# Optimization experiments

Measured on AMD Instinct MI355X. Metric: run time of the kernel, lower is better.

The kernel has to match this reference:

```python
import math
import jax, jax.numpy as jnp
import numpy as np

N_HEADS = 16

def setup_inputs() -> dict:
    key = jax.random.key(0)
    qkv = jax.random.normal(key, (4, 3072, 2048), dtype=jnp.float32)
    return {"qkv": qkv}

def reference(qkv):
    bs, width, length = qkv.shape
    ch = width // (3 * N_HEADS)
    # [bs*H, 3*ch, L] -> split into q, k, v of [bs*H, ch, L]
    qkv_r = qkv.reshape(bs * N_HEADS, 3 * ch, length)
    q, k, v = qkv_r[:, :ch], qkv_r[:, ch:2 * ch], qkv_r[:, 2 * ch:]
    scale = 1.0 / math.sqrt(math.sqrt(ch))
    # scores: [bs*H, T, S]
    weight = jnp.einsum('bct,bcs->bts', q * scale, k * scale)
    weight = jax.nn.softmax(weight, axis=-1)
    a = jnp.einsum('bts,bcs->bct', weight, v)
    return a.reshape(bs, -1, length)
```

## Files before the change

kernel.cpp:

```cpp
#include <hip/hip_runtime.h>
#include <cstdint>

typedef _Float16 half8 __attribute__((ext_vector_type(8)));
typedef __fp16 fp16x2 __attribute__((ext_vector_type(2)));
typedef float f32x4 __attribute__((ext_vector_type(4)));

#define HSTRIDE 131072
#define KOFF    ((size_t)64 * HSTRIDE)
#define VOFF    ((size_t)128 * HSTRIDE)

__device__ __forceinline__ float fast_exp2(float x) {
    return __builtin_amdgcn_exp2f(x);
}

__device__ __forceinline__ uint32_t pkrtz(float a, float b) {
    fp16x2 h = __builtin_amdgcn_cvt_pkrtz(a, b);
    return __builtin_bit_cast(uint32_t, h);
}

__device__ __forceinline__ void load_lds16(const _Float16* g, _Float16* l) {
    auto* g1 = reinterpret_cast<const __attribute__((address_space(1))) uint32_t*>(
        reinterpret_cast<uintptr_t>(g));
    auto* l3 = reinterpret_cast<__attribute__((address_space(3))) uint32_t*>(
        reinterpret_cast<uintptr_t>(l));
    __builtin_amdgcn_global_load_lds(g1, l3, 16, 0, 0);
}

__global__ __launch_bounds__(256) void prep_kernel(const float* __restrict__ qkv,
                                                   _Float16* __restrict__ ws)
{
    __shared__ float Lf[64 * 132];

    const int tid = threadIdx.x;
    const int bid = blockIdx.x;
    const float kQ = 0.125f * 1.44269504088896340736f;

    if (bid < 2048) {
        const int type  = bid >> 10;
        const int head  = (bid >> 4) & 63;
        const int chunk = bid & 15;
        const int b4 = head >> 4, h = head & 15;
        const float* src = qkv + (((size_t)(b4 * 3072 + h * 192 + type * 64)) << 11)
                         + chunk * 128;

#pragma unroll
        for (int k = 0; k < 8; ++k) {
            int idx = k * 256 + tid;
            int c = idx >> 5;
            int t4 = (idx & 31) << 2;
            *(float4*)&Lf[c * 132 + t4] = *(const float4*)&src[((size_t)c << 11) + t4];
        }
        __syncthreads();

        const int tl = tid >> 1;
        const int gh = (tid & 1) * 4;
        const float scale = (type == 0) ? kQ : 1.0f;
        const int row = chunk * 128 + tl;
        const size_t rowbase = ((type == 0) ? (size_t)head * HSTRIDE
                                            : KOFF + (size_t)head * HSTRIDE)
                             + (size_t)row * 64;
#pragma unroll
        for (int gg = 0; gg < 4; ++gg) {
            const int g = gh + gg;
            uint32_t d[4];
#pragma unroll
            for (int j = 0; j < 4; ++j) {
                float a = Lf[(8 * g + 2 * j) * 132 + tl];
                float b = Lf[(8 * g + 2 * j + 1) * 132 + tl];
                d[j] = pkrtz(a * scale, b * scale);
            }
            const int pos = (type == 0) ? g : (g ^ (tl & 7));
            *(uint4*)&ws[rowbase + ((size_t)pos << 3)] = make_uint4(d[0], d[1], d[2], d[3]);
        }
    } else {
        const int vb = bid - 2048;
        const int head = vb >> 4, chunk = vb & 15;
        const int b4 = head >> 4, h = head & 15;
        const float* src = qkv + (((size_t)(b4 * 3072 + h * 192 + 128)) << 11) + chunk * 128;
#pragma unroll
        for (int k = 0; k < 4; ++k) {
            const int c  = k * 16 + (tid >> 4);
            const int gs = tid & 15;
            const float* p = &src[((size_t)c << 11) + gs * 8];
            float4 f0 = *(const float4*)&p[0];
            float4 f1 = *(const float4*)&p[4];
            uint32_t d0 = pkrtz(f0.x, f0.y);
            uint32_t d1 = pkrtz(f0.z, f0.w);
            uint32_t d2 = pkrtz(f1.x, f1.y);
            uint32_t d3 = pkrtz(f1.z, f1.w);
            size_t o = VOFF + (size_t)head * HSTRIDE + (size_t)chunk * 8192
                     + ((size_t)c << 7) + (size_t)((gs ^ (c & 15)) << 3);
            *(uint4*)&ws[o] = make_uint4(d0, d1, d2, d3);
        }
    }
}

__launch_bounds__(256, 2)
__global__ void attn_kernel(const _Float16* __restrict__ ws, float* __restrict__ out)
{
    __shared__ __align__(16) _Float16 sK[128 * 64];
    __shared__ __align__(16) _Float16 sV[64 * 128];
    __shared__ __align__(16) _Float16 sP[128 * 128];
    __shared__ float sL[4][32];

    const int tid  = threadIdx.x;
    const int lane = tid & 63;
    const int wave = tid >> 6;
    const int l15  = lane & 15;
    const int quad = lane >> 4;

    const int bid  = blockIdx.x;
    const int head = bid & 63;
    const int tblk = bid >> 6;
    const int T0   = tblk * 128;
    const int b4   = head >> 4;
    const int h    = head & 15;

    const _Float16* Qt = ws + (size_t)head * HSTRIDE;
    const _Float16* Kt = ws + KOFF + (size_t)head * HSTRIDE;
    const _Float16* Vt = ws + VOFF + (size_t)head * HSTRIDE;

    half8 qb[2][2];
#pragma unroll
    for (int nt = 0; nt < 2; ++nt)
#pragma unroll
        for (int ks = 0; ks < 2; ++ks)
            qb[nt][ks] = *(const half8*)&Qt[(size_t)(T0 + wave * 32 + nt * 16 + l15) * 64
                                            + ks * 32 + quad * 8];

    int kb[2];
#pragma unroll
    for (int ks = 0; ks < 2; ++ks)
        kb[ks] = l15 * 64 + (((ks * 4 + quad) ^ (l15 & 7)) << 3);
    int vbs[4], pb[4];
#pragma unroll
    for (int ks = 0; ks < 4; ++ks) {
        vbs[ks] = l15 * 128 + (((ks * 4 + quad) ^ l15) << 3);
        pb[ks]  = (wave * 32 + l15) * 128 + (((ks * 4 + quad) ^ l15) << 3);
    }
    int pw[8];
#pragma unroll
    for (int mt = 0; mt < 8; ++mt)
        pw[mt] = (wave * 32 + l15) * 128
               + ((((2 * mt + (quad >> 1)) ^ l15) << 3) + ((quad & 1) << 2));

    f32x4 Oacc[2][4];
#pragma unroll
    for (int nt = 0; nt < 2; ++nt)
#pragma unroll
        for (int ct = 0; ct < 4; ++ct) Oacc[nt][ct] = (f32x4)0.f;
    float lacc[2] = {0.f, 0.f};
    const f32x4 fz = (f32x4)0.f;

    for (int it = 0; it < 16; ++it) {
        __syncthreads();
        const _Float16* kg = Kt + (size_t)it * 8192;
        const _Float16* vg = Vt + (size_t)it * 8192;
#pragma unroll
        for (int i = 0; i < 4; ++i) {
            int off = (i * 4 + wave) * 512;
            load_lds16(kg + off + lane * 8, &sK[off]);
            load_lds16(vg + off + lane * 8, &sV[off]);
        }
        __syncthreads();

        f32x4 Sc[8][2];
#pragma unroll
        for (int mt = 0; mt < 8; ++mt) {
            half8 ka0 = *(const half8*)&sK[kb[0] + mt * 1024];
            half8 ka1 = *(const half8*)&sK[kb[1] + mt * 1024];
#pragma unroll
            for (int nt = 0; nt < 2; ++nt) {
                f32x4 c0 = __builtin_amdgcn_mfma_f32_16x16x32_f16(ka0, qb[nt][0], fz, 0, 0, 0);
                Sc[mt][nt] = __builtin_amdgcn_mfma_f32_16x16x32_f16(ka1, qb[nt][1], c0, 0, 0, 0);
            }
        }

#pragma unroll
        for (int mt = 0; mt < 8; ++mt)
#pragma unroll
            for (int nt = 0; nt < 2; ++nt) {
                f32x4 s = Sc[mt][nt];
                float p0 = fast_exp2(s[0]);
                float p1 = fast_exp2(s[1]);
                float p2 = fast_exp2(s[2]);
                float p3 = fast_exp2(s[3]);
                lacc[nt] += p0; lacc[nt] += p1; lacc[nt] += p2; lacc[nt] += p3;
                uint32_t w0 = pkrtz(p0, p1);
                uint32_t w1 = pkrtz(p2, p3);
                *(uint2*)&sP[pw[mt] + nt * 2048] = make_uint2(w0, w1);
            }

        half8 pa[2][4];
#pragma unroll
        for (int nt = 0; nt < 2; ++nt)
#pragma unroll
            for (int ks = 0; ks < 4; ++ks)
                pa[nt][ks] = *(const half8*)&sP[pb[ks] + nt * 2048];
#pragma unroll
        for (int ct = 0; ct < 4; ++ct) {
#pragma unroll
            for (int ks = 0; ks < 4; ++ks) {
                half8 vbf = *(const half8*)&sV[vbs[ks] + ct * 2048];
                Oacc[0][ct] = __builtin_amdgcn_mfma_f32_16x16x32_f16(pa[0][ks], vbf, Oacc[0][ct], 0, 0, 0);
                Oacc[1][ct] = __builtin_amdgcn_mfma_f32_16x16x32_f16(pa[1][ks], vbf, Oacc[1][ct], 0, 0, 0);
            }
        }
    }

#pragma unroll
    for (int nt = 0; nt < 2; ++nt) {
        float v = lacc[nt];
        v += __shfl_xor(v, 16, 64);
        v += __shfl_xor(v, 32, 64);
        if (quad == 0) sL[wave][nt * 16 + l15] = v;
    }
    __builtin_amdgcn_s_waitcnt(0);
    float inv[2][4];
#pragma unroll
    for (int nt = 0; nt < 2; ++nt)
#pragma unroll
        for (int r = 0; r < 4; ++r)
            inv[nt][r] = 1.f / sL[wave][nt * 16 + quad * 4 + r];

    float* ob = out + (((size_t)(b4 * 1024 + h * 64)) << 11) + T0 + wave * 32;
#pragma unroll
    for (int nt = 0; nt < 2; ++nt)
#pragma unroll
        for (int ct = 0; ct < 4; ++ct) {
            f32x4 o = Oacc[nt][ct];
#pragma unroll
            for (int r = 0; r < 4; ++r) o[r] *= inv[nt][r];
            *(f32x4*)&ob[((size_t)(ct * 16 + l15) << 11) + nt * 16 + quad * 4] = o;
        }
}

extern "C" void kernel_launch(void* const* d_in, const int* in_sizes, int n_in,
                              void* d_out, int out_size, void* d_ws, size_t ws_size,
                              hipStream_t stream) {
    const float* qkv = (const float*)d_in[0];
    float* out = (float*)d_out;
    _Float16* ws = (_Float16*)d_ws;
    prep_kernel<<<dim3(3072), dim3(256), 0, stream>>>(qkv, ws);
    attn_kernel<<<dim3(1024), dim3(256), 0, stream>>>(ws, out);
}
```

Baseline: 252.0 us.

## Double-buffer 64-key K/V tiles in LDS and shrink tiles for higher occupancy

Splits each 128-key iteration into two 64-key halves with double-buffered K and V LDS tiles, so the async global-to-LDS load of the next tile overlaps compute on the current one. The V workspace layout is reorganised into 64-key chunks with a new swizzle to match. The P buffer is halved and read back via two 8-byte loads per fragment. Launch bounds are raised to 3 blocks per CU, now that LDS use is smaller. This trades extra barriers and smaller MFMA batches per barrier for latency hiding and occupancy, at the risk of register spills.

```diff
diff --git a/kernel.cpp b/kernel.cpp
--- a/kernel.cpp
+++ b/kernel.cpp
@@ -88,19 +88,21 @@
             uint32_t d1 = pkrtz(f0.z, f0.w);
             uint32_t d2 = pkrtz(f1.x, f1.y);
             uint32_t d3 = pkrtz(f1.z, f1.w);
-            size_t o = VOFF + (size_t)head * HSTRIDE + (size_t)chunk * 8192
-                     + ((size_t)c << 7) + (size_t)((gs ^ (c & 15)) << 3);
+            const int sch = chunk * 2 + (gs >> 3);
+            const int gsl = gs & 7;
+            size_t o = VOFF + (size_t)head * HSTRIDE + (size_t)sch * 4096
+                     + ((size_t)c << 6) + (size_t)((gsl ^ (c & 7)) << 3);
             *(uint4*)&ws[o] = make_uint4(d0, d1, d2, d3);
         }
     }
 }
 
-__launch_bounds__(256, 2)
+__launch_bounds__(256, 3)
 __global__ void attn_kernel(const _Float16* __restrict__ ws, float* __restrict__ out)
 {
-    __shared__ __align__(16) _Float16 sK[128 * 64];
-    __shared__ __align__(16) _Float16 sV[64 * 128];
-    __shared__ __align__(16) _Float16 sP[128 * 128];
+    __shared__ __align__(16) _Float16 sK[2][4096];
+    __shared__ __align__(16) _Float16 sV[2][4096];
+    __shared__ __align__(16) _Float16 sP[128 * 64];
     __shared__ float sL[4][32];
 
     const int tid  = threadIdx.x;
@@ -128,21 +130,23 @@
             qb[nt][ks] = *(const half8*)&Qt[(size_t)(T0 + wave * 32 + nt * 16 + l15) * 64
                                             + ks * 32 + quad * 8];
 
-    int kb[2];
-#pragma unroll
-    for (int ks = 0; ks < 2; ++ks)
-        kb[ks] = l15 * 64 + (((ks * 4 + quad) ^ (l15 & 7)) << 3);
-    int vbs[4], pb[4];
-#pragma unroll
-    for (int ks = 0; ks < 4; ++ks) {
-        vbs[ks] = l15 * 128 + (((ks * 4 + quad) ^ l15) << 3);
-        pb[ks]  = (wave * 32 + l15) * 128 + (((ks * 4 + quad) ^ l15) << 3);
-    }
-    int pw[8];
-#pragma unroll
-    for (int mt = 0; mt < 8; ++mt)
-        pw[mt] = (wave * 32 + l15) * 128
-               + ((((2 * mt + (quad >> 1)) ^ l15) << 3) + ((quad & 1) << 2));
+    int kb[2], vbs[2];
+#pragma unroll
+    for (int ks = 0; ks < 2; ++ks) {
+        kb[ks]  = l15 * 64 + (((ks * 4 + quad) ^ (l15 & 7)) << 3);
+        vbs[ks] = l15 * 64 + (((ks * 4 + quad) ^ (l15 & 7)) << 3);
+    }
+    const int prow = (wave * 32 + l15) * 64;
+    int pu[4];
+#pragma unroll
+    for (int i = 0; i < 4; ++i) {
+        int ks = i >> 1, e = i & 1;
+        pu[i] = prow + ((((ks << 3) + (quad << 1) + e) ^ l15) << 2);
+    }
+    int pwb[4];
+#pragma unroll
+    for (int mt = 0; mt < 4; ++mt)
+        pwb[mt] = prow + ((((mt << 2) + quad) ^ l15) << 2);
 
     f32x4 Oacc[2][4];
 #pragma unroll
@@ -152,58 +156,75 @@
     float lacc[2] = {0.f, 0.f};
     const f32x4 fz = (f32x4)0.f;
 
-    for (int it = 0; it < 16; ++it) {
-        __syncthreads();
-        const _Float16* kg = Kt + (size_t)it * 8192;
-        const _Float16* vg = Vt + (size_t)it * 8192;
-#pragma unroll
-        for (int i = 0; i < 4; ++i) {
-            int off = (i * 4 + wave) * 512;
-            load_lds16(kg + off + lane * 8, &sK[off]);
-            load_lds16(vg + off + lane * 8, &sV[off]);
-        }
-        __syncthreads();
-
-        f32x4 Sc[8][2];
-#pragma unroll
-        for (int mt = 0; mt < 8; ++mt) {
-            half8 ka0 = *(const half8*)&sK[kb[0] + mt * 1024];
-            half8 ka1 = *(const half8*)&sK[kb[1] + mt * 1024];
-#pragma unroll
-            for (int nt = 0; nt < 2; ++nt) {
-                f32x4 c0 = __builtin_amdgcn_mfma_f32_16x16x32_f16(ka0, qb[nt][0], fz, 0, 0, 0);
-                Sc[mt][nt] = __builtin_amdgcn_mfma_f32_16x16x32_f16(ka1, qb[nt][1], c0, 0, 0, 0);
-            }
-        }
-
-#pragma unroll
-        for (int mt = 0; mt < 8; ++mt)
-#pragma unroll
-            for (int nt = 0; nt < 2; ++nt) {
-                f32x4 s = Sc[mt][nt];
-                float p0 = fast_exp2(s[0]);
-                float p1 = fast_exp2(s[1]);
-                float p2 = fast_exp2(s[2]);
-                float p3 = fast_exp2(s[3]);
-                lacc[nt] += p0; lacc[nt] += p1; lacc[nt] += p2; lacc[nt] += p3;
-                uint32_t w0 = pkrtz(p0, p1);
-                uint32_t w1 = pkrtz(p2, p3);
-                *(uint2*)&sP[pw[mt] + nt * 2048] = make_uint2(w0, w1);
-            }
-
-        half8 pa[2][4];
-#pragma unroll
-        for (int nt = 0; nt < 2; ++nt)
-#pragma unroll
-            for (int ks = 0; ks < 4; ++ks)
-                pa[nt][ks] = *(const half8*)&sP[pb[ks] + nt * 2048];
-#pragma unroll
-        for (int ct = 0; ct < 4; ++ct) {
-#pragma unroll
-            for (int ks = 0; ks < 4; ++ks) {
-                half8 vbf = *(const half8*)&sV[vbs[ks] + ct * 2048];
-                Oacc[0][ct] = __builtin_amdgcn_mfma_f32_16x16x32_f16(pa[0][ks], vbf, Oacc[0][ct], 0, 0, 0);
-                Oacc[1][ct] = __builtin_amdgcn_mfma_f32_16x16x32_f16(pa[1][ks], vbf, Oacc[1][ct], 0, 0, 0);
+    auto stage = [&](int buf, int tile) {
+        const _Float16* kg = Kt + (size_t)tile * 4096 + wave * 1024 + lane * 8;
+        const _Float16* vg = Vt + (size_t)tile * 4096 + wave * 1024 + lane * 8;
+        _Float16* kd = &sK[buf][wave * 1024];
+        _Float16* vd = &sV[buf][wave * 1024];
+        load_lds16(kg,       kd);
+        load_lds16(kg + 512, kd + 512);
+        load_lds16(vg,       vd);
+        load_lds16(vg + 512, vd + 512);
+    };
+
+    stage(0, 0);
+
+    for (int itp = 0; itp < 16; ++itp) {
+#pragma unroll
+        for (int hf = 0; hf < 2; ++hf) {
+            const int it = 2 * itp + hf;
+            __syncthreads();
+            if (hf == 0) {
+                stage(1, it + 1);
+            } else if (itp + 1 < 16) {
+                stage(0, it + 1);
+            }
+            const _Float16* sKb = sK[hf];
+            const _Float16* sVb = sV[hf];
+
+            f32x4 Sc[4][2];
+#pragma unroll
+            for (int mt = 0; mt < 4; ++mt) {
+                half8 ka0 = *(const half8*)&sKb[kb[0] + mt * 1024];
+                half8 ka1 = *(const half8*)&sKb[kb[1] + mt * 1024];
+#pragma unroll
+                for (int nt = 0; nt < 2; ++nt) {
+                    f32x4 c0 = __builtin_amdgcn_mfma_f32_16x16x32_f16(ka0, qb[nt][0], fz, 0, 0, 0);
+                    Sc[mt][nt] = __builtin_amdgcn_mfma_f32_16x16x32_f16(ka1, qb[nt][1], c0, 0, 0, 0);
+                }
+            }
+
+#pragma unroll
+            for (int mt = 0; mt < 4; ++mt)
+#pragma unroll
+                for (int nt = 0; nt < 2; ++nt) {
+                    f32x4 s = Sc[mt][nt];
+                    float p0 = fast_exp2(s[0]);
+                    float p1 = fast_exp2(s[1]);
+                    float p2 = fast_exp2(s[2]);
+                    float p3 = fast_exp2(s[3]);
+                    lacc[nt] += p0; lacc[nt] += p1; lacc[nt] += p2; lacc[nt] += p3;
+                    *(uint2*)&sP[pwb[mt] + nt * 1024] = make_uint2(pkrtz(p0, p1), pkrtz(p2, p3));
+                }
+
+            half8 pa[2][2];
+#pragma unroll
+            for (int nt = 0; nt < 2; ++nt)
+#pragma unroll
+                for (int ks = 0; ks < 2; ++ks) {
+                    uint2 lo = *(const uint2*)&sP[pu[ks * 2 + 0] + nt * 1024];
+                    uint2 hi = *(const uint2*)&sP[pu[ks * 2 + 1] + nt * 1024];
+                    pa[nt][ks] = __builtin_bit_cast(half8, make_uint4(lo.x, lo.y, hi.x, hi.y));
+                }
+
+#pragma unroll
+            for (int ct = 0; ct < 4; ++ct) {
+#pragma unroll
+                for (int ks = 0; ks < 2; ++ks) {
+                    half8 vbf = *(const half8*)&sVb[vbs[ks] + ct * 1024];
+                    Oacc[0][ct] = __builtin_amdgcn_mfma_f32_16x16x32_f16(pa[0][ks], vbf, Oacc[0][ct], 0, 0, 0);
+                    Oacc[1][ct] = __builtin_amdgcn_mfma_f32_16x16x32_f16(pa[1][ks], vbf, Oacc[1][ct], 0, 0, 0);
+                }
             }
         }
     }
```

After: 243.6 us. -3.3%, faster.

## Keep softmax probabilities in registers and triple-buffer K/V tiles in attention

Applied to the files above, without the earlier changes.

Prep now writes K and V into an MFMA-fragment-ordered layout so the attention kernel can load operands with linear lane offsets. Attention feeds the S accumulator outputs directly as the B operand of the PV MFMA, which removes the sP shared-memory round trip and its barrier. K/V tiles shrink to 64 keys and are triple-buffered with asynchronous global-to-LDS loads. Each block now covers 256 queries with 64 per wave, giving more Q reuse. The tradeoffs are higher register pressure and scalar, less coalesced output stores.

```diff
diff --git a/kernel.cpp b/kernel.cpp
--- a/kernel.cpp
+++ b/kernel.cpp
@@ -29,68 +29,73 @@
 __global__ __launch_bounds__(256) void prep_kernel(const float* __restrict__ qkv,
                                                    _Float16* __restrict__ ws)
 {
-    __shared__ float Lf[64 * 132];
+    __shared__ float Lf[64 * 66];
 
     const int tid = threadIdx.x;
     const int bid = blockIdx.x;
     const float kQ = 0.125f * 1.44269504088896340736f;
 
-    if (bid < 2048) {
-        const int type  = bid >> 10;
-        const int head  = (bid >> 4) & 63;
-        const int chunk = bid & 15;
+    if (bid < 4096) {
+        const int type  = bid >> 11;
+        const int head  = (bid >> 5) & 63;
+        const int chunk = bid & 31;
         const int b4 = head >> 4, h = head & 15;
         const float* src = qkv + (((size_t)(b4 * 3072 + h * 192 + type * 64)) << 11)
-                         + chunk * 128;
-
-#pragma unroll
-        for (int k = 0; k < 8; ++k) {
+                         + chunk * 64;
+
+#pragma unroll
+        for (int k = 0; k < 4; ++k) {
             int idx = k * 256 + tid;
-            int c = idx >> 5;
-            int t4 = (idx & 31) << 2;
-            *(float4*)&Lf[c * 132 + t4] = *(const float4*)&src[((size_t)c << 11) + t4];
+            int c = idx >> 4;
+            int t4 = (idx & 15) << 2;
+            float4 f = *(const float4*)&src[(((size_t)c) << 11) + t4];
+            *(float2*)&Lf[c * 66 + t4]     = make_float2(f.x, f.y);
+            *(float2*)&Lf[c * 66 + t4 + 2] = make_float2(f.z, f.w);
         }
         __syncthreads();
 
-        const int tl = tid >> 1;
-        const int gh = (tid & 1) * 4;
         const float scale = (type == 0) ? kQ : 1.0f;
-        const int row = chunk * 128 + tl;
-        const size_t rowbase = ((type == 0) ? (size_t)head * HSTRIDE
-                                            : KOFF + (size_t)head * HSTRIDE)
-                             + (size_t)row * 64;
-#pragma unroll
-        for (int gg = 0; gg < 4; ++gg) {
-            const int g = gh + gg;
+#pragma unroll
+        for (int k = 0; k < 2; ++k) {
+            const int g  = (tid >> 6) + 4 * k;
+            const int tl = tid & 63;
             uint32_t d[4];
 #pragma unroll
             for (int j = 0; j < 4; ++j) {
-                float a = Lf[(8 * g + 2 * j) * 132 + tl];
-                float b = Lf[(8 * g + 2 * j + 1) * 132 + tl];
+                float a = Lf[(8 * g + 2 * j) * 66 + tl];
+                float b = Lf[(8 * g + 2 * j + 1) * 66 + tl];
                 d[j] = pkrtz(a * scale, b * scale);
             }
-            const int pos = (type == 0) ? g : (g ^ (tl & 7));
-            *(uint4*)&ws[rowbase + ((size_t)pos << 3)] = make_uint4(d[0], d[1], d[2], d[3]);
+            size_t off;
+            if (type == 0) {
+                off = (size_t)head * HSTRIDE + (size_t)(chunk * 64 + tl) * 64 + g * 8;
+            } else {
+                const int st = chunk * 4 + (tl >> 4);
+                off = KOFF + (size_t)head * HSTRIDE
+                    + (size_t)((st * 2 + (g >> 2)) * 512)
+                    + (size_t)(((g & 3) * 16 + (tl & 15)) * 8);
+            }
+            *(uint4*)&ws[off] = make_uint4(d[0], d[1], d[2], d[3]);
         }
     } else {
-        const int vb = bid - 2048;
-        const int head = vb >> 4, chunk = vb & 15;
+        const int vb = bid - 4096;
+        const int head = vb >> 5, chunk = vb & 31;
         const int b4 = head >> 4, h = head & 15;
-        const float* src = qkv + (((size_t)(b4 * 3072 + h * 192 + 128)) << 11) + chunk * 128;
-#pragma unroll
-        for (int k = 0; k < 4; ++k) {
-            const int c  = k * 16 + (tid >> 4);
-            const int gs = tid & 15;
-            const float* p = &src[((size_t)c << 11) + gs * 8];
+        const float* src = qkv + (((size_t)(b4 * 3072 + h * 192 + 128)) << 11) + chunk * 64;
+#pragma unroll
+        for (int k = 0; k < 2; ++k) {
+            const int u = k * 256 + tid;
+            const int q = u & 3;
+            const int c = (u >> 2) & 63;
+            const int sc_l = u >> 8;
+            const float* p = &src[((size_t)c << 11) + sc_l * 32 + q * 4];
             float4 f0 = *(const float4*)&p[0];
-            float4 f1 = *(const float4*)&p[4];
-            uint32_t d0 = pkrtz(f0.x, f0.y);
-            uint32_t d1 = pkrtz(f0.z, f0.w);
-            uint32_t d2 = pkrtz(f1.x, f1.y);
-            uint32_t d3 = pkrtz(f1.z, f1.w);
-            size_t o = VOFF + (size_t)head * HSTRIDE + (size_t)chunk * 8192
-                     + ((size_t)c << 7) + (size_t)((gs ^ (c & 15)) << 3);
-            *(uint4*)&ws[o] = make_uint4(d0, d1, d2, d3);
+            float4 f1 = *(const float4*)&p[16];
+            size_t off = VOFF + (size_t)head * HSTRIDE
+                       + (size_t)((((chunk * 2 + sc_l) * 4) + (c >> 4)) * 512)
+                       + (size_t)((q * 16 + (c & 15)) * 8);
+            *(uint4*)&ws[off] = make_uint4(pkrtz(f0.x, f0.y), pkrtz(f0.z, f0.w),
+                                           pkrtz(f1.x, f1.y), pkrtz(f1.z, f1.w));
         }
     }
 }
@@ -98,10 +103,8 @@
 __launch_bounds__(256, 2)
 __global__ void attn_kernel(const _Float16* __restrict__ ws, float* __restrict__ out)
 {
-    __shared__ __align__(16) _Float16 sK[128 * 64];
-    __shared__ __align__(16) _Float16 sV[64 * 128];
-    __shared__ __align__(16) _Float16 sP[128 * 128];
-    __shared__ float sL[4][32];
+    __shared__ __align__(16) _Float16 sK[3][4096];
+    __shared__ __align__(16) _Float16 sV[3][4096];
 
     const int tid  = threadIdx.x;
     const int lane = tid & 63;
@@ -112,7 +115,7 @@
     const int bid  = blockIdx.x;
     const int head = bid & 63;
     const int tblk = bid >> 6;
-    const int T0   = tblk * 128;
+    const int T0   = tblk * 256;
     const int b4   = head >> 4;
     const int h    = head & 15;
 
@@ -120,118 +123,112 @@
     const _Float16* Kt = ws + KOFF + (size_t)head * HSTRIDE;
     const _Float16* Vt = ws + VOFF + (size_t)head * HSTRIDE;
 
-    half8 qb[2][2];
-#pragma unroll
-    for (int nt = 0; nt < 2; ++nt)
+    half8 qb[4][2];
+#pragma unroll
+    for (int nt = 0; nt < 4; ++nt)
 #pragma unroll
         for (int ks = 0; ks < 2; ++ks)
-            qb[nt][ks] = *(const half8*)&Qt[(size_t)(T0 + wave * 32 + nt * 16 + l15) * 64
+            qb[nt][ks] = *(const half8*)&Qt[(size_t)(T0 + wave * 64 + nt * 16 + l15) * 64
                                             + ks * 32 + quad * 8];
 
-    int kb[2];
-#pragma unroll
-    for (int ks = 0; ks < 2; ++ks)
-        kb[ks] = l15 * 64 + (((ks * 4 + quad) ^ (l15 & 7)) << 3);
-    int vbs[4], pb[4];
-#pragma unroll
-    for (int ks = 0; ks < 4; ++ks) {
-        vbs[ks] = l15 * 128 + (((ks * 4 + quad) ^ l15) << 3);
-        pb[ks]  = (wave * 32 + l15) * 128 + (((ks * 4 + quad) ^ l15) << 3);
+    f32x4 Oacc[4][4];
+#pragma unroll
+    for (int ct = 0; ct < 4; ++ct)
+#pragma unroll
+        for (int nt = 0; nt < 4; ++nt) Oacc[ct][nt] = (f32x4)0.f;
+    float lacc[4] = {0.f, 0.f, 0.f, 0.f};
+    const f32x4 fz = (f32x4)0.f;
+
+    auto stage = [&](int buf, int tile) {
+        const _Float16* kg = Kt + (size_t)tile * 4096 + wave * 1024 + lane * 8;
+        const _Float16* vg = Vt + (size_t)tile * 4096 + wave * 1024 + lane * 8;
+        load_lds16(kg,       &sK[buf][wave * 1024]);
+        load_lds16(kg + 512, &sK[buf][wave * 1024 + 512]);
+        load_lds16(vg,       &sV[buf][wave * 1024]);
+        load_lds16(vg + 512, &sV[buf][wave * 1024 + 512]);
+    };
+
+    stage(0, 0);
+
+    int cur = 0, nxt = 1;
+    for (int it = 0; it < 32; ++it) {
+        __builtin_amdgcn_s_waitcnt(0);
+        __syncthreads();
+        if (it < 31) stage(nxt, it + 1);
+        const _Float16* sKb = sK[cur];
+        const _Float16* sVb = sV[cur];
+        cur = nxt; nxt = (nxt == 2) ? 0 : nxt + 1;
+        const int lb = lane * 8;
+
+        half8 kf[4][2];
+#pragma unroll
+        for (int mt = 0; mt < 4; ++mt)
+#pragma unroll
+            for (int ks = 0; ks < 2; ++ks)
+                kf[mt][ks] = *(const half8*)&sKb[(mt * 2 + ks) * 512 + lb];
+
+        half8 pf[2][4];
+#pragma unroll
+        for (int sc2 = 0; sc2 < 2; ++sc2) {
+            f32x4 Sa[4], Sb[4];
+#pragma unroll
+            for (int nt = 0; nt < 4; ++nt) {
+                f32x4 t0 = __builtin_amdgcn_mfma_f32_16x16x32_f16(kf[2 * sc2][0], qb[nt][0], fz, 0, 0, 0);
+                Sa[nt]   = __builtin_amdgcn_mfma_f32_16x16x32_f16(kf[2 * sc2][1], qb[nt][1], t0, 0, 0, 0);
+                f32x4 t1 = __builtin_amdgcn_mfma_f32_16x16x32_f16(kf[2 * sc2 + 1][0], qb[nt][0], fz, 0, 0, 0);
+                Sb[nt]   = __builtin_amdgcn_mfma_f32_16x16x32_f16(kf[2 * sc2 + 1][1], qb[nt][1], t1, 0, 0, 0);
+            }
+#pragma unroll
+            for (int nt = 0; nt < 4; ++nt) {
+                float e0 = fast_exp2(Sa[nt][0]);
+                float e1 = fast_exp2(Sa[nt][1]);
+                float e2 = fast_exp2(Sa[nt][2]);
+                float e3 = fast_exp2(Sa[nt][3]);
+                float e4 = fast_exp2(Sb[nt][0]);
+                float e5 = fast_exp2(Sb[nt][1]);
+                float e6 = fast_exp2(Sb[nt][2]);
+                float e7 = fast_exp2(Sb[nt][3]);
+                lacc[nt] += ((e0 + e1) + (e2 + e3)) + ((e4 + e5) + (e6 + e7));
+                uint4 u = make_uint4(pkrtz(e0, e1), pkrtz(e2, e3),
+                                     pkrtz(e4, e5), pkrtz(e6, e7));
+                pf[sc2][nt] = __builtin_bit_cast(half8, u);
+            }
+        }
+
+        half8 vf[2][4];
+#pragma unroll
+        for (int sc2 = 0; sc2 < 2; ++sc2)
+#pragma unroll
+            for (int ct = 0; ct < 4; ++ct)
+                vf[sc2][ct] = *(const half8*)&sVb[(sc2 * 4 + ct) * 512 + lb];
+#pragma unroll
+        for (int ct = 0; ct < 4; ++ct)
+#pragma unroll
+            for (int sc2 = 0; sc2 < 2; ++sc2)
+#pragma unroll
+                for (int nt = 0; nt < 4; ++nt)
+                    Oacc[ct][nt] = __builtin_amdgcn_mfma_f32_16x16x32_f16(
+                        vf[sc2][ct], pf[sc2][nt], Oacc[ct][nt], 0, 0, 0);
     }
-    int pw[8];
-#pragma unroll
-    for (int mt = 0; mt < 8; ++mt)
-        pw[mt] = (wave * 32 + l15) * 128
-               + ((((2 * mt + (quad >> 1)) ^ l15) << 3) + ((quad & 1) << 2));
-
-    f32x4 Oacc[2][4];
-#pragma unroll
-    for (int nt = 0; nt < 2; ++nt)
-#pragma unroll
-        for (int ct = 0; ct < 4; ++ct) Oacc[nt][ct] = (f32x4)0.f;
-    float lacc[2] = {0.f, 0.f};
-    const f32x4 fz = (f32x4)0.f;
-
-    for (int it = 0; it < 16; ++it) {
-        __syncthreads();
-        const _Float16* kg = Kt + (size_t)it * 8192;
-        const _Float16* vg = Vt + (size_t)it * 8192;
-#pragma unroll
-        for (int i = 0; i < 4; ++i) {
-            int off = (i * 4 + wave) * 512;
-            load_lds16(kg + off + lane * 8, &sK[off]);
-            load_lds16(vg + off + lane * 8, &sV[off]);
-        }
-        __syncthreads();
-
-        f32x4 Sc[8][2];
-#pragma unroll
-        for (int mt = 0; mt < 8; ++mt) {
-            half8 ka0 = *(const half8*)&sK[kb[0] + mt * 1024];
-            half8 ka1 = *(const half8*)&sK[kb[1] + mt * 1024];
-#pragma unroll
-            for (int nt = 0; nt < 2; ++nt) {
-                f32x4 c0 = __builtin_amdgcn_mfma_f32_16x16x32_f16(ka0, qb[nt][0], fz, 0, 0, 0);
-                Sc[mt][nt] = __builtin_amdgcn_mfma_f32_16x16x32_f16(ka1, qb[nt][1], c0, 0, 0, 0);
-            }
-        }
-
-#pragma unroll
-        for (int mt = 0; mt < 8; ++mt)
-#pragma unroll
-            for (int nt = 0; nt < 2; ++nt) {
-                f32x4 s = Sc[mt][nt];
-                float p0 = fast_exp2(s[0]);
-                float p1 = fast_exp2(s[1]);
-                float p2 = fast_exp2(s[2]);
-                float p3 = fast_exp2(s[3]);
-                lacc[nt] += p0; lacc[nt] += p1; lacc[nt] += p2; lacc[nt] += p3;
-                uint32_t w0 = pkrtz(p0, p1);
-                uint32_t w1 = pkrtz(p2, p3);
-                *(uint2*)&sP[pw[mt] + nt * 2048] = make_uint2(w0, w1);
-            }
-
-        half8 pa[2][4];
-#pragma unroll
-        for (int nt = 0; nt < 2; ++nt)
-#pragma unroll
-            for (int ks = 0; ks < 4; ++ks)
-                pa[nt][ks] = *(const half8*)&sP[pb[ks] + nt * 2048];
-#pragma unroll
-        for (int ct = 0; ct < 4; ++ct) {
-#pragma unroll
-            for (int ks = 0; ks < 4; ++ks) {
-                half8 vbf = *(const half8*)&sV[vbs[ks] + ct * 2048];
-                Oacc[0][ct] = __builtin_amdgcn_mfma_f32_16x16x32_f16(pa[0][ks], vbf, Oacc[0][ct], 0, 0, 0);
-                Oacc[1][ct] = __builtin_amdgcn_mfma_f32_16x16x32_f16(pa[1][ks], vbf, Oacc[1][ct], 0, 0, 0);
-            }
-        }
-    }
-
-#pragma unroll
-    for (int nt = 0; nt < 2; ++nt) {
+
+    float inv[4];
+#pragma unroll
+    for (int nt = 0; nt < 4; ++nt) {
         float v = lacc[nt];
         v += __shfl_xor(v, 16, 64);
         v += __shfl_xor(v, 32, 64);
-        if (quad == 0) sL[wave][nt * 16 + l15] = v;
+        inv[nt] = 1.f / v;
     }
-    __builtin_amdgcn_s_waitcnt(0);
-    float inv[2][4];
-#pragma unroll
-    for (int nt = 0; nt < 2; ++nt)
-#pragma unroll
-        for (int r = 0; r < 4; ++r)
-            inv[nt][r] = 1.f / sL[wave][nt * 16 + quad * 4 + r];
-
-    float* ob = out + (((size_t)(b4 * 1024 + h * 64)) << 11) + T0 + wave * 32;
-#pragma unroll
-    for (int nt = 0; nt < 2; ++nt)
-#pragma unroll
-        for (int ct = 0; ct < 4; ++ct) {
-            f32x4 o = Oacc[nt][ct];
-#pragma unroll
-            for (int r = 0; r < 4; ++r) o[r] *= inv[nt][r];
-            *(f32x4*)&ob[((size_t)(ct * 16 + l15) << 11) + nt * 16 + quad * 4] = o;
+
+    float* ob = out + (((size_t)(b4 * 1024 + h * 64)) << 11) + T0 + wave * 64;
+#pragma unroll
+    for (int ct = 0; ct < 4; ++ct)
+#pragma unroll
+        for (int nt = 0; nt < 4; ++nt) {
+            f32x4 o = Oacc[ct][nt];
+#pragma unroll
+            for (int r = 0; r < 4; ++r)
+                ob[((size_t)(ct * 16 + quad * 4 + r) << 11) + nt * 16 + l15] = o[r] * inv[nt];
         }
 }
 
@@ -241,6 +238,6 @@
     const float* qkv = (const float*)d_in[0];
     float* out = (float*)d_out;
     _Float16* ws = (_Float16*)d_ws;
-    prep_kernel<<<dim3(3072), dim3(256), 0, stream>>>(qkv, ws);
-    attn_kernel<<<dim3(1024), dim3(256), 0, stream>>>(ws, out);
-}
+    prep_kernel<<<dim3(6144), dim3(256), 0, stream>>>(qkv, ws);
+    attn_kernel<<<dim3(512), dim3(256), 0, stream>>>(ws, out);
+}
```

Result: faster. 227.1 us (-9.9%).
